# Performance work log

Hardware: AMD Instinct MI355X
Metric: run time of the kernel (lower is better)

## Reference

```python
import jax, jax.numpy as jnp
import numpy as np

# NOBlock config: no_dims_in=(8,8), input_dim=output_dim=128, rank=8, level_diff=1
B, N, V = 4, 2048, 1
G1, G2, C = 8, 8, 128   # in_shape = (8, 8, 128); m = G1*G2 = 64 grid cells per token
M = G1 * G2
R = 8                    # Tucker ranks: [8, 8, 8] in and out (min(dim, rank))
LEVEL_DIFF = 1
GRP = 4 ** LEVEL_DIFF    # quadtree group size for hierarchical residual


def _xavier(key, shape):
    lim = float(np.sqrt(6.0 / (shape[0] + shape[1])))
    return jax.random.uniform(key, shape, jnp.float32, -lim, lim)


def setup_inputs() -> dict:
    key = jax.random.key(0)
    ks = jax.random.split(key, 10)
    x = jax.random.normal(ks[0], (B, N, V, M, C), jnp.float32)
    # core ~ N(0, scale^2), scale = sqrt(2/(fan_in+fan_out)), fan = prod(ranks) = 8^3
    scale = float(np.sqrt(2.0 / (R ** 3 + R ** 3)))
    core = jax.random.normal(ks[1], (R, R, R, R, R, R), jnp.float32) * scale
    out_f0 = _xavier(ks[2], (G1, R))
    out_f1 = _xavier(ks[3], (G2, R))
    out_f2 = _xavier(ks[4], (C, R))
    in_f0 = _xavier(ks[5], (G1, R))
    in_f1 = _xavier(ks[6], (G2, R))
    in_f2 = _xavier(ks[7], (C, R))
    mask = jax.random.bernoulli(ks[8], 0.25, (B, N, M))  # True = masked cell
    return {"x": x, "core": core, "out_f0": out_f0, "out_f1": out_f1,
            "out_f2": out_f2, "in_f0": in_f0, "in_f1": in_f1, "in_f2": in_f2,
            "mask": mask}


def reference(x, core, out_f0, out_f1, out_f2, in_f0, in_f1, in_f2, mask):
    b, n, v = x.shape[:3]
    # --- CrossTuckerLayer: 'bnvade,ABCDEF,oA,pB,qC,aD,dE,eF->bnvopq' ---
    xr = x.reshape(b, n, v, G1, G2, C)
    # project onto in-factor rank spaces
    z = jnp.einsum('bnvade,aD,dE,eF->bnvDEF', xr, in_f0, in_f1, in_f2, optimize=True)
    # core contraction (out-ranks ABC x in-ranks DEF)
    z = jnp.einsum('bnvDEF,ABCDEF->bnvABC', z, core)
    # expand to output dims
    h = jnp.einsum('bnvABC,oA,pB,qC->bnvopq', z, out_f0, out_f1, out_f2, optimize=True)
    h = h.reshape(b, n, v, M, C)
    # residual connection
    h = h + x
    # --- get_residual: hierarchical masked mixing, level_diff = 1 ---
    h4 = h.reshape(b, n * v, M, C)                     # v = 1
    hg = h4.reshape(b, -1, GRP, M, C)                  # [b, n/4, 4, m, c]
    w = (~mask).reshape(b, -1, GRP, M, 1).sum(axis=2, keepdims=True).astype(h.dtype)
    out = (hg / (w + 1e-10)).sum(axis=2)               # [b, n/4, m, c]
    out = out * (w.sum(axis=2) != 0).astype(h.dtype)
    return out
```

## Files before the change

### kernel.cpp

```cpp
#include <hip/hip_runtime.h>
#include <cstdint>
#include <cstddef>


__device__ __forceinline__ float dot4(const float4 a, const float4 b, float s) {
    return fmaf(a.w, b.w, fmaf(a.z, b.z, fmaf(a.y, b.y, fmaf(a.x, b.x, s))));
}

__device__ __forceinline__ unsigned f2bf_pk(float lo, float hi) {
    unsigned ul = __float_as_uint(lo), uh = __float_as_uint(hi);
    ul += 0x7FFFu + ((ul >> 16) & 1u);
    uh += 0x7FFFu + ((uh >> 16) & 1u);
    return (ul >> 16) | (uh & 0xFFFF0000u);
}

__launch_bounds__(256, 4)
__global__ void k1_inproj(const float* __restrict__ x,
                          const float* __restrict__ core,
                          float* __restrict__ coreT,
                          const float* __restrict__ if0,
                          const float* __restrict__ if1,
                          const float* __restrict__ if2,
                          unsigned* __restrict__ xsum_bf,
                          float* __restrict__ zz_ws)
{
    __shared__ float xs[64 * 132];
    __shared__ float s_if2T[8 * 132];
    __shared__ float s_if0[64], s_if1[64];
    float* t1 = xs;
    float* t2 = xs + 512;

    const int t = threadIdx.x;
    const int blk = blockIdx.x;

    if (blk < 64) {
        const int tid = blk * 256 + t;
        const float4* c4 = (const float4*)core;
        float4* cT4 = (float4*)coreT;
        #pragma unroll
        for (int q = 0; q < 4; ++q) {
            const int idx = tid + 16384 * q;
            const int r = idx & 511, k4 = idx >> 9;
            cT4[(size_t)k4 * 512 + r] = c4[(size_t)r * 128 + k4];
        }
        return;
    }
    const int g = blk - 64;

    for (int i = t; i < 1024; i += 256) {
        const int e = i & 127, F = i >> 7;
        s_if2T[F * 132 + e] = if2[e * 8 + F];
    }
    if (t < 64) { s_if0[t] = if0[t]; s_if1[t] = if1[t]; }

    const float4* xg4 = (const float4*)(x + (size_t)g * 4 * 8192);
    float4 acc[8];
    #pragma unroll
    for (int i = 0; i < 8; ++i) acc[i] = xg4[t + 256 * i];
    #pragma unroll
    for (int j = 1; j < 4; ++j) {
        float4 v[8];
        #pragma unroll
        for (int i = 0; i < 8; ++i) v[i] = xg4[(size_t)j * 2048 + t + 256 * i];
        #pragma unroll
        for (int i = 0; i < 8; ++i) {
            acc[i].x += v[i].x; acc[i].y += v[i].y;
            acc[i].z += v[i].z; acc[i].w += v[i].w;
        }
    }
    uint2* xo = (uint2*)xsum_bf + (size_t)g * 2048;
    #pragma unroll
    for (int i = 0; i < 8; ++i) {
        uint2 pk;
        pk.x = f2bf_pk(acc[i].x, acc[i].y);
        pk.y = f2bf_pk(acc[i].z, acc[i].w);
        xo[t + 256 * i] = pk;
    }
    #pragma unroll
    for (int i = 0; i < 8; ++i) {
        const int f4i = t + 256 * i;
        *(float4*)&xs[(f4i >> 5) * 132 + (f4i & 31) * 4] = acc[i];
    }
    __syncthreads();

    float r0, r1;
    #pragma unroll
    for (int h = 0; h < 2; ++h) {
        const int id = t + 256 * h;
        const int m = id >> 3, F = id & 7;
        const float4* xr = (const float4*)(xs + m * 132);
        const float4* wr = (const float4*)(s_if2T + F * 132);
        float s0 = 0.f, s1 = 0.f;
        #pragma unroll
        for (int e4 = 0; e4 < 32; e4 += 2) {
            s0 = dot4(xr[e4],     wr[e4],     s0);
            s1 = dot4(xr[e4 + 1], wr[e4 + 1], s1);
        }
        if (h == 0) r0 = s0 + s1; else r1 = s0 + s1;
    }
    __syncthreads();
    t1[t] = r0;
    t1[t + 256] = r1;
    __syncthreads();

    #pragma unroll
    for (int h = 0; h < 2; ++h) {
        const int id = t + 256 * h;
        const int E = id >> 6, a = (id >> 3) & 7, F = id & 7;
        float s = 0.f;
        #pragma unroll
        for (int d0 = 0; d0 < 8; ++d0) {
            const int d = (d0 + a) & 7;
            s = fmaf(t1[a * 64 + d * 8 + F], s_if1[d * 8 + E], s);
        }
        t2[id] = s;
    }
    __syncthreads();

    #pragma unroll
    for (int h = 0; h < 2; ++h) {
        const int id = t + 256 * h;
        const int D = id >> 6, E = (id >> 3) & 7, F = id & 7;
        float s = 0.f;
        #pragma unroll
        for (int a0 = 0; a0 < 8; ++a0) {
            const int a = (a0 + E) & 7;
            s = fmaf(t2[E * 64 + a * 8 + F], s_if0[a * 8 + D], s);
        }
        zz_ws[(size_t)g * 512 + id] = s;
    }
}

__launch_bounds__(512, 2)
__global__ void k2_core_outproj(const float* __restrict__ coreT,
                                const float* __restrict__ zz_ws,
                                const unsigned* __restrict__ xsum_bf,
                                const float* __restrict__ of0,
                                const float* __restrict__ of1,
                                const float* __restrict__ of2,
                                const int* __restrict__ mask,
                                float* __restrict__ out)
{
    __shared__ float zz[2048];
    __shared__ float z2[2048];
    __shared__ float s_of0T[64], s_of1T[64];
    __shared__ float s_winv[256];
    float* t1 = zz;
    float* t2 = z2;

    const int t = threadIdx.x;
    const size_t g0 = (size_t)blockIdx.x * 4;

    ((float4*)zz)[t] = ((const float4*)(zz_ws + g0 * 512))[t];
    if (t < 64) {
        s_of0T[t] = of0[(t & 7) * 8 + (t >> 3)];
        s_of1T[t] = of1[(t & 7) * 8 + (t >> 3)];
    }
    if (t < 256) {
        const int g = t >> 6, m = t & 63;
        const int* mp = mask + (g0 + g) * 4 * 64 + m;
        int cnt = 0;
        #pragma unroll
        for (int j = 0; j < 4; ++j) cnt += (mp[j * 64] == 0) ? 1 : 0;
        s_winv[t] = cnt ? 1.0f / (float)cnt : 0.0f;
    }
    __syncthreads();

    {
        const float4* cT = (const float4*)coreT;
        const float4* z4 = (const float4*)zz;
        float a0[4] = {0, 0, 0, 0}, a1[4] = {0, 0, 0, 0};
        for (int k4 = 0; k4 < 128; k4 += 2) {
            const float4 c0 = cT[(size_t)k4 * 512 + t];
            const float4 c1 = cT[(size_t)(k4 + 1) * 512 + t];
            #pragma unroll
            for (int g = 0; g < 4; ++g) {
                a0[g] = dot4(c0, z4[g * 128 + k4],     a0[g]);
                a1[g] = dot4(c1, z4[g * 128 + k4 + 1], a1[g]);
            }
        }
        #pragma unroll
        for (int g = 0; g < 4; ++g) z2[g * 512 + t] = a0[g] + a1[g];
    }
    __syncthreads();

    #pragma unroll
    for (int h = 0; h < 4; ++h) {
        const int id2 = t + 512 * h;
        const int g = id2 >> 9, rem = id2 & 511;
        const int o = rem >> 6, Bq = (rem >> 3) & 7, Cr = rem & 7;
        float s = 0.f;
        #pragma unroll
        for (int A = 0; A < 8; ++A)
            s = fmaf(z2[g * 512 + A * 64 + Bq * 8 + Cr], s_of0T[A * 8 + o], s);
        t1[id2] = s;
    }
    __syncthreads();

    #pragma unroll
    for (int h = 0; h < 4; ++h) {
        const int id2 = t + 512 * h;
        const int g = id2 >> 9, rem = id2 & 511;
        const int p = rem >> 6, o = (rem >> 3) & 7, Cr = rem & 7;
        float s = 0.f;
        #pragma unroll
        for (int B0 = 0; B0 < 8; ++B0) {
            const int Bq = (B0 + o) & 7;
            s = fmaf(t1[g * 512 + o * 64 + Bq * 8 + Cr], s_of1T[Bq * 8 + p], s);
        }
        t2[id2] = s;
    }
    __syncthreads();

    float4 w[4][2];
    {
        const int cc = (4 * t) & 127;
        #pragma unroll
        for (int c = 0; c < 4; ++c) {
            w[c][0] = *(const float4*)(of2 + (cc + c) * 8);
            w[c][1] = *(const float4*)(of2 + (cc + c) * 8 + 4);
        }
    }
    float4* out4 = (float4*)out;
    #pragma unroll
    for (int g = 0; g < 4; ++g) {
        const size_t obase = (g0 + g) * 2048;
        const uint2* xb = (const uint2*)xsum_bf + obase;
        uint2 xp[4];
        #pragma unroll
        for (int i = 0; i < 4; ++i) xp[i] = xb[t + 512 * i];
        #pragma unroll
        for (int i = 0; i < 4; ++i) {
            const int m = (t >> 5) + 16 * i;
            const int o = m >> 3, p = m & 7;
            const float wv = s_winv[g * 64 + m];
            const int base = g * 512 + p * 64 + o * 8;
            const float4 v0 = *(const float4*)(t2 + base);
            const float4 v1 = *(const float4*)(t2 + base + 4);
            const float rx = __uint_as_float(xp[i].x << 16);
            const float ry = __uint_as_float(xp[i].x & 0xFFFF0000u);
            const float rz = __uint_as_float(xp[i].y << 16);
            const float rw = __uint_as_float(xp[i].y & 0xFFFF0000u);
            float4 r;
            r.x = dot4(v1, w[0][1], dot4(v0, w[0][0], rx));
            r.y = dot4(v1, w[1][1], dot4(v0, w[1][0], ry));
            r.z = dot4(v1, w[2][1], dot4(v0, w[2][0], rz));
            r.w = dot4(v1, w[3][1], dot4(v0, w[3][0], rw));
            r.x *= wv; r.y *= wv; r.z *= wv; r.w *= wv;
            out4[obase + t + 512 * i] = r;
        }
    }
}

__launch_bounds__(256, 3)
__global__ void noblock_fused(const float* __restrict__ x,
                              const float* __restrict__ core,
                              const float* __restrict__ of0,
                              const float* __restrict__ of1,
                              const float* __restrict__ of2,
                              const float* __restrict__ if0,
                              const float* __restrict__ if1,
                              const float* __restrict__ if2,
                              const int* __restrict__ mask,
                              float* __restrict__ out)
{
    __shared__ float xs[64 * 132];
    __shared__ float t1[512];
    __shared__ float t2[512];
    __shared__ float zz[2 * 512];
    __shared__ float z2[2 * 512];
    __shared__ float s_if2T[8 * 132];
    __shared__ float s_if0[64], s_if1[64];
    __shared__ float s_of0T[64], s_of1T[64];
    __shared__ float s_winv[128];

    const int t = threadIdx.x;
    const int blk = blockIdx.x;

    for (int i = t; i < 1024; i += 256) {
        const int e = i & 127, F = i >> 7;
        s_if2T[F * 132 + e] = if2[e * 8 + F];
    }
    if (t < 64) {
        s_if0[t] = if0[t];
        s_if1[t] = if1[t];
        s_of0T[t] = of0[(t & 7) * 8 + (t >> 3)];
        s_of1T[t] = of1[(t & 7) * 8 + (t >> 3)];
    }
    if (t < 128) {
        const int g = t >> 6, mm = t & 63;
        const int* mp = mask + ((size_t)(blk * 2 + g) * 4) * 64 + mm;
        int cnt = 0;
        #pragma unroll
        for (int j = 0; j < 4; ++j) cnt += (mp[j * 64] == 0) ? 1 : 0;
        s_winv[t] = cnt ? 1.0f / (float)cnt : 0.0f;
    }

    float4 acc[2][8];
    const float4* xg4 = (const float4*)(x + (size_t)blk * 8 * 8192);
    #pragma unroll
    for (int g = 0; g < 2; ++g)
        #pragma unroll
        for (int i = 0; i < 8; ++i)
            acc[g][i] = xg4[(size_t)(g * 4) * 2048 + t + 256 * i];
    #pragma unroll
    for (int j = 1; j < 4; ++j) {
        #pragma unroll
        for (int g = 0; g < 2; ++g) {
            float4 v[8];
            #pragma unroll
            for (int i = 0; i < 8; ++i)
                v[i] = xg4[(size_t)(g * 4 + j) * 2048 + t + 256 * i];
            #pragma unroll
            for (int i = 0; i < 8; ++i) {
                acc[g][i].x += v[i].x; acc[g][i].y += v[i].y;
                acc[g][i].z += v[i].z; acc[g][i].w += v[i].w;
            }
        }
    }

    #pragma unroll
    for (int g = 0; g < 2; ++g) {
        #pragma unroll
        for (int i = 0; i < 8; ++i) {
            const int f4i = t + 256 * i;
            *(float4*)&xs[(f4i >> 5) * 132 + (f4i & 31) * 4] = acc[g][i];
        }
        __syncthreads();
        #pragma unroll
        for (int h = 0; h < 2; ++h) {
            const int id = t + 256 * h;
            const int m = id >> 3, F = id & 7;
            const float4* xr = (const float4*)(xs + m * 132);
            const float4* wr = (const float4*)(s_if2T + F * 132);
            float s0 = 0.f, s1 = 0.f;
            #pragma unroll
            for (int e4 = 0; e4 < 32; e4 += 2) {
                s0 = dot4(xr[e4],     wr[e4],     s0);
                s1 = dot4(xr[e4 + 1], wr[e4 + 1], s1);
            }
            t1[id] = s0 + s1;
        }
        __syncthreads();
        #pragma unroll
        for (int h = 0; h < 2; ++h) {
            const int id = t + 256 * h;
            const int E = id >> 6, a = (id >> 3) & 7, F = id & 7;
            float s = 0.f;
            #pragma unroll
            for (int d0 = 0; d0 < 8; ++d0) {
                const int d = (d0 + a) & 7;
                s = fmaf(t1[a * 64 + d * 8 + F], s_if1[d * 8 + E], s);
            }
            t2[id] = s;
        }
        __syncthreads();
        #pragma unroll
        for (int h = 0; h < 2; ++h) {
            const int id = t + 256 * h;
            const int D = id >> 6, E = (id >> 3) & 7, F = id & 7;
            float s = 0.f;
            #pragma unroll
            for (int a0 = 0; a0 < 8; ++a0) {
                const int a = (a0 + E) & 7;
                s = fmaf(t2[E * 64 + a * 8 + F], s_if0[a * 8 + D], s);
            }
            zz[g * 512 + id] = s;
        }
        __syncthreads();
    }

    {
        const float4* cr0 = (const float4*)(core + (size_t)t * 512);
        const float4* cr1 = (const float4*)(core + (size_t)(t + 256) * 512);
        const float4* z4 = (const float4*)zz;
        float a0[2] = {0.f, 0.f}, a1[2] = {0.f, 0.f};
        for (int kk = 0; kk < 128; ++kk) {
            const float4 c0 = cr0[kk], c1 = cr1[kk];
            #pragma unroll
            for (int g = 0; g < 2; ++g) {
                const float4 zv = z4[g * 128 + kk];
                a0[g] = dot4(c0, zv, a0[g]);
                a1[g] = dot4(c1, zv, a1[g]);
            }
        }
        #pragma unroll
        for (int g = 0; g < 2; ++g) {
            z2[g * 512 + t]       = a0[g];
            z2[g * 512 + t + 256] = a1[g];
        }
    }
    __syncthreads();

    float4 w[4][2];
    {
        const int cc = (4 * t) & 127;
        #pragma unroll
        for (int c = 0; c < 4; ++c) {
            w[c][0] = *(const float4*)(of2 + (cc + c) * 8);
            w[c][1] = *(const float4*)(of2 + (cc + c) * 8 + 4);
        }
    }

    float4* out4 = (float4*)out;
    #pragma unroll
    for (int g = 0; g < 2; ++g) {
        #pragma unroll
        for (int h = 0; h < 2; ++h) {
            const int id = t + 256 * h;
            const int o = id >> 6, Bq = (id >> 3) & 7, Cr = id & 7;
            float s = 0.f;
            #pragma unroll
            for (int A = 0; A < 8; ++A)
                s = fmaf(z2[g * 512 + A * 64 + Bq * 8 + Cr], s_of0T[A * 8 + o], s);
            t1[id] = s;
        }
        __syncthreads();
        #pragma unroll
        for (int h = 0; h < 2; ++h) {
            const int id = t + 256 * h;
            const int p = id >> 6, o = (id >> 3) & 7, Cr = id & 7;
            float s = 0.f;
            #pragma unroll
            for (int B0 = 0; B0 < 8; ++B0) {
                const int Bq = (B0 + o) & 7;
                s = fmaf(t1[o * 64 + Bq * 8 + Cr], s_of1T[Bq * 8 + p], s);
            }
            t2[id] = s;
        }
        __syncthreads();
        #pragma unroll
        for (int i = 0; i < 8; ++i) {
            const int m = (t >> 5) + 8 * i;
            const int o = m >> 3, p = m & 7;
            const float wv = s_winv[g * 64 + m];
            const int base = p * 64 + o * 8;
            const float4 v0 = *(const float4*)(t2 + base);
            const float4 v1 = *(const float4*)(t2 + base + 4);
            float4 r;
            r.x = dot4(v1, w[0][1], dot4(v0, w[0][0], acc[g][i].x));
            r.y = dot4(v1, w[1][1], dot4(v0, w[1][0], acc[g][i].y));
            r.z = dot4(v1, w[2][1], dot4(v0, w[2][0], acc[g][i].z));
            r.w = dot4(v1, w[3][1], dot4(v0, w[3][0], acc[g][i].w));
            r.x *= wv; r.y *= wv; r.z *= wv; r.w *= wv;
            out4[(size_t)(blk * 2 + g) * 2048 + t + 256 * i] = r;
        }
        __syncthreads();
    }
}

extern "C" void kernel_launch(void* const* d_in, const int* in_sizes, int n_in,
                              void* d_out, int out_size, void* d_ws, size_t ws_size,
                              hipStream_t stream) {
    const float* x    = (const float*)d_in[0];
    const float* core = (const float*)d_in[1];
    const float* of0  = (const float*)d_in[2];
    const float* of1  = (const float*)d_in[3];
    const float* of2  = (const float*)d_in[4];
    const float* if0  = (const float*)d_in[5];
    const float* if1  = (const float*)d_in[6];
    const float* if2  = (const float*)d_in[7];
    const int* mask   = (const int*)d_in[8];
    float* out = (float*)d_out;

    const size_t CORE_T_BYTES = (size_t)512 * 512 * 4;
    const size_t ZZ_BYTES     = (size_t)2048 * 512 * 4;
    const size_t XS_BYTES     = (size_t)2048 * 8192 * 2;

    if (d_ws && ws_size >= CORE_T_BYTES + ZZ_BYTES + XS_BYTES) {
        float* coreT    = (float*)d_ws;
        float* zz_ws    = (float*)((char*)d_ws + CORE_T_BYTES);
        unsigned* xs_bf = (unsigned*)((char*)d_ws + CORE_T_BYTES + ZZ_BYTES);
        k1_inproj<<<dim3(2112), dim3(256), 0, stream>>>(
            x, core, coreT, if0, if1, if2, xs_bf, zz_ws);
        k2_core_outproj<<<dim3(512), dim3(512), 0, stream>>>(
            coreT, zz_ws, xs_bf, of0, of1, of2, mask, out);
    } else {
        noblock_fused<<<dim3(1024), dim3(256), 0, stream>>>(
            x, core, of0, of1, of2, if0, if1, if2, mask, out);
    }
}
```

Measured before the change: 111.8 us.

## Fuse input projection into core/output kernel, split core transpose into its own launch

The input-projection stage (x group sum, bf16 residual store, Tucker in-projection) moves into the main kernel. Each 512-thread block now processes its 4 groups sequentially into shared memory, so the zz intermediate no longer round-trips through global memory. Core transposition becomes a tiny separate kernel. The trade-off is a loop of 4 groups with several syncs per group inside one block, and grid-level parallelism for the x reads drops from 2048 blocks to 512 blocks, which could reduce memory-level parallelism.

New measurement: 107.6 us. 3.8% less time.

```diff
diff --git a/kernel.cpp b/kernel.cpp
--- a/kernel.cpp
+++ b/kernel.cpp
@@ -14,145 +14,49 @@
     return (ul >> 16) | (uh & 0xFFFF0000u);
 }
 
-__launch_bounds__(256, 4)
-__global__ void k1_inproj(const float* __restrict__ x,
-                          const float* __restrict__ core,
-                          float* __restrict__ coreT,
-                          const float* __restrict__ if0,
-                          const float* __restrict__ if1,
-                          const float* __restrict__ if2,
-                          unsigned* __restrict__ xsum_bf,
-                          float* __restrict__ zz_ws)
+__global__ void transpose_core(const float* __restrict__ core,
+                               float* __restrict__ coreT) {
+    const int tid = blockIdx.x * 256 + threadIdx.x;
+    const int r = tid & 511, k4 = tid >> 9;
+    ((float4*)coreT)[(size_t)k4 * 512 + r] =
+        ((const float4*)core)[(size_t)r * 128 + k4];
+}
+
+__launch_bounds__(512, 2)
+__global__ void noblock_main(const float* __restrict__ x,
+                             const float* __restrict__ coreT,
+                             const float* __restrict__ of0,
+                             const float* __restrict__ of1,
+                             const float* __restrict__ of2,
+                             const float* __restrict__ if0,
+                             const float* __restrict__ if1,
+                             const float* __restrict__ if2,
+                             const int* __restrict__ mask,
+                             unsigned* __restrict__ xsum_bf,
+                             float* __restrict__ out)
 {
     __shared__ float xs[64 * 132];
+    __shared__ float zz[2048];
+    __shared__ float z2[2048];
     __shared__ float s_if2T[8 * 132];
     __shared__ float s_if0[64], s_if1[64];
+    __shared__ float s_of0T[64], s_of1T[64];
+    __shared__ float s_winv[256];
     float* t1 = xs;
     float* t2 = xs + 512;
+    float* t1d = zz;
+    float* t2d = z2;
 
     const int t = threadIdx.x;
-    const int blk = blockIdx.x;
-
-    if (blk < 64) {
-        const int tid = blk * 256 + t;
-        const float4* c4 = (const float4*)core;
-        float4* cT4 = (float4*)coreT;
-        #pragma unroll
-        for (int q = 0; q < 4; ++q) {
-            const int idx = tid + 16384 * q;
-            const int r = idx & 511, k4 = idx >> 9;
-            cT4[(size_t)k4 * 512 + r] = c4[(size_t)r * 128 + k4];
-        }
-        return;
-    }
-    const int g = blk - 64;
-
-    for (int i = t; i < 1024; i += 256) {
+    const size_t g0 = (size_t)blockIdx.x * 4;
+
+    for (int i = t; i < 1024; i += 512) {
         const int e = i & 127, F = i >> 7;
         s_if2T[F * 132 + e] = if2[e * 8 + F];
     }
-    if (t < 64) { s_if0[t] = if0[t]; s_if1[t] = if1[t]; }
-
-    const float4* xg4 = (const float4*)(x + (size_t)g * 4 * 8192);
-    float4 acc[8];
-    #pragma unroll
-    for (int i = 0; i < 8; ++i) acc[i] = xg4[t + 256 * i];
-    #pragma unroll
-    for (int j = 1; j < 4; ++j) {
-        float4 v[8];
-        #pragma unroll
-        for (int i = 0; i < 8; ++i) v[i] = xg4[(size_t)j * 2048 + t + 256 * i];
-        #pragma unroll
-        for (int i = 0; i < 8; ++i) {
-            acc[i].x += v[i].x; acc[i].y += v[i].y;
-            acc[i].z += v[i].z; acc[i].w += v[i].w;
-        }
-    }
-    uint2* xo = (uint2*)xsum_bf + (size_t)g * 2048;
-    #pragma unroll
-    for (int i = 0; i < 8; ++i) {
-        uint2 pk;
-        pk.x = f2bf_pk(acc[i].x, acc[i].y);
-        pk.y = f2bf_pk(acc[i].z, acc[i].w);
-        xo[t + 256 * i] = pk;
-    }
-    #pragma unroll
-    for (int i = 0; i < 8; ++i) {
-        const int f4i = t + 256 * i;
-        *(float4*)&xs[(f4i >> 5) * 132 + (f4i & 31) * 4] = acc[i];
-    }
-    __syncthreads();
-
-    float r0, r1;
-    #pragma unroll
-    for (int h = 0; h < 2; ++h) {
-        const int id = t + 256 * h;
-        const int m = id >> 3, F = id & 7;
-        const float4* xr = (const float4*)(xs + m * 132);
-        const float4* wr = (const float4*)(s_if2T + F * 132);
-        float s0 = 0.f, s1 = 0.f;
-        #pragma unroll
-        for (int e4 = 0; e4 < 32; e4 += 2) {
-            s0 = dot4(xr[e4],     wr[e4],     s0);
-            s1 = dot4(xr[e4 + 1], wr[e4 + 1], s1);
-        }
-        if (h == 0) r0 = s0 + s1; else r1 = s0 + s1;
-    }
-    __syncthreads();
-    t1[t] = r0;
-    t1[t + 256] = r1;
-    __syncthreads();
-
-    #pragma unroll
-    for (int h = 0; h < 2; ++h) {
-        const int id = t + 256 * h;
-        const int E = id >> 6, a = (id >> 3) & 7, F = id & 7;
-        float s = 0.f;
-        #pragma unroll
-        for (int d0 = 0; d0 < 8; ++d0) {
-            const int d = (d0 + a) & 7;
-            s = fmaf(t1[a * 64 + d * 8 + F], s_if1[d * 8 + E], s);
-        }
-        t2[id] = s;
-    }
-    __syncthreads();
-
-    #pragma unroll
-    for (int h = 0; h < 2; ++h) {
-        const int id = t + 256 * h;
-        const int D = id >> 6, E = (id >> 3) & 7, F = id & 7;
-        float s = 0.f;
-        #pragma unroll
-        for (int a0 = 0; a0 < 8; ++a0) {
-            const int a = (a0 + E) & 7;
-            s = fmaf(t2[E * 64 + a * 8 + F], s_if0[a * 8 + D], s);
-        }
-        zz_ws[(size_t)g * 512 + id] = s;
-    }
-}
-
-__launch_bounds__(512, 2)
-__global__ void k2_core_outproj(const float* __restrict__ coreT,
-                                const float* __restrict__ zz_ws,
-                                const unsigned* __restrict__ xsum_bf,
-                                const float* __restrict__ of0,
-                                const float* __restrict__ of1,
-                                const float* __restrict__ of2,
-                                const int* __restrict__ mask,
-                                float* __restrict__ out)
-{
-    __shared__ float zz[2048];
-    __shared__ float z2[2048];
-    __shared__ float s_of0T[64], s_of1T[64];
-    __shared__ float s_winv[256];
-    float* t1 = zz;
-    float* t2 = z2;
-
-    const int t = threadIdx.x;
-    const size_t g0 = (size_t)blockIdx.x * 4;
-
-    ((float4*)zz)[t] = ((const float4*)(zz_ws + g0 * 512))[t];
     if (t < 64) {
+        s_if0[t] = if0[t];
+        s_if1[t] = if1[t];
         s_of0T[t] = of0[(t & 7) * 8 + (t >> 3)];
         s_of1T[t] = of1[(t & 7) * 8 + (t >> 3)];
     }
@@ -164,7 +68,80 @@
         for (int j = 0; j < 4; ++j) cnt += (mp[j * 64] == 0) ? 1 : 0;
         s_winv[t] = cnt ? 1.0f / (float)cnt : 0.0f;
     }
-    __syncthreads();
+
+    #pragma unroll 1
+    for (int g = 0; g < 4; ++g) {
+        const float4* xg4 = (const float4*)x + (g0 + g) * 8192;
+        float4 v[4][4];
+        #pragma unroll
+        for (int j = 0; j < 4; ++j)
+            #pragma unroll
+            for (int i = 0; i < 4; ++i)
+                v[j][i] = xg4[(size_t)j * 2048 + t + 512 * i];
+        float4 acc[4];
+        #pragma unroll
+        for (int i = 0; i < 4; ++i) {
+            acc[i].x = (v[0][i].x + v[1][i].x) + (v[2][i].x + v[3][i].x);
+            acc[i].y = (v[0][i].y + v[1][i].y) + (v[2][i].y + v[3][i].y);
+            acc[i].z = (v[0][i].z + v[1][i].z) + (v[2][i].z + v[3][i].z);
+            acc[i].w = (v[0][i].w + v[1][i].w) + (v[2][i].w + v[3][i].w);
+        }
+        uint2* xo = (uint2*)xsum_bf + (g0 + g) * 2048;
+        #pragma unroll
+        for (int i = 0; i < 4; ++i) {
+            uint2 pk;
+            pk.x = f2bf_pk(acc[i].x, acc[i].y);
+            pk.y = f2bf_pk(acc[i].z, acc[i].w);
+            xo[t + 512 * i] = pk;
+        }
+        #pragma unroll
+        for (int i = 0; i < 4; ++i) {
+            const int f4i = t + 512 * i;
+            *(float4*)&xs[(f4i >> 5) * 132 + (f4i & 31) * 4] = acc[i];
+        }
+        __syncthreads();
+
+        float r0;
+        {
+            const int m = t >> 3, F = t & 7;
+            const float4* xr = (const float4*)(xs + m * 132);
+            const float4* wr = (const float4*)(s_if2T + F * 132);
+            float s0 = 0.f, s1 = 0.f;
+            #pragma unroll
+            for (int e4 = 0; e4 < 32; e4 += 2) {
+                s0 = dot4(xr[e4],     wr[e4],     s0);
+                s1 = dot4(xr[e4 + 1], wr[e4 + 1], s1);
+            }
+            r0 = s0 + s1;
+        }
+        __syncthreads();
+        t1[t] = r0;
+        __syncthreads();
+
+        {
+            const int E = t >> 6, a = (t >> 3) & 7, F = t & 7;
+            float s = 0.f;
+            #pragma unroll
+            for (int d0 = 0; d0 < 8; ++d0) {
+                const int d = (d0 + a) & 7;
+                s = fmaf(t1[a * 64 + d * 8 + F], s_if1[d * 8 + E], s);
+            }
+            t2[t] = s;
+        }
+        __syncthreads();
+
+        {
+            const int D = t >> 6, E = (t >> 3) & 7, F = t & 7;
+            float s = 0.f;
+            #pragma unroll
+            for (int a0 = 0; a0 < 8; ++a0) {
+                const int a = (a0 + E) & 7;
+                s = fmaf(t2[E * 64 + a * 8 + F], s_if0[a * 8 + D], s);
+            }
+            zz[g * 512 + t] = s;
+        }
+        __syncthreads();
+    }
 
     {
         const float4* cT = (const float4*)coreT;
@@ -193,7 +170,7 @@
         #pragma unroll
         for (int A = 0; A < 8; ++A)
             s = fmaf(z2[g * 512 + A * 64 + Bq * 8 + Cr], s_of0T[A * 8 + o], s);
-        t1[id2] = s;
+        t1d[id2] = s;
     }
     __syncthreads();
 
@@ -206,9 +183,9 @@
         #pragma unroll
         for (int B0 = 0; B0 < 8; ++B0) {
             const int Bq = (B0 + o) & 7;
-            s = fmaf(t1[g * 512 + o * 64 + Bq * 8 + Cr], s_of1T[Bq * 8 + p], s);
-        }
-        t2[id2] = s;
+            s = fmaf(t1d[g * 512 + o * 64 + Bq * 8 + Cr], s_of1T[Bq * 8 + p], s);
+        }
+        t2d[id2] = s;
     }
     __syncthreads();
 
@@ -235,8 +212,8 @@
             const int o = m >> 3, p = m & 7;
             const float wv = s_winv[g * 64 + m];
             const int base = g * 512 + p * 64 + o * 8;
-            const float4 v0 = *(const float4*)(t2 + base);
-            const float4 v1 = *(const float4*)(t2 + base + 4);
+            const float4 v0 = *(const float4*)(t2d + base);
+            const float4 v1 = *(const float4*)(t2d + base + 4);
             const float rx = __uint_as_float(xp[i].x << 16);
             const float ry = __uint_as_float(xp[i].x & 0xFFFF0000u);
             const float rz = __uint_as_float(xp[i].y << 16);
@@ -464,17 +441,14 @@
     float* out = (float*)d_out;
 
     const size_t CORE_T_BYTES = (size_t)512 * 512 * 4;
-    const size_t ZZ_BYTES     = (size_t)2048 * 512 * 4;
     const size_t XS_BYTES     = (size_t)2048 * 8192 * 2;
 
-    if (d_ws && ws_size >= CORE_T_BYTES + ZZ_BYTES + XS_BYTES) {
+    if (d_ws && ws_size >= CORE_T_BYTES + XS_BYTES) {
         float* coreT    = (float*)d_ws;
-        float* zz_ws    = (float*)((char*)d_ws + CORE_T_BYTES);
-        unsigned* xs_bf = (unsigned*)((char*)d_ws + CORE_T_BYTES + ZZ_BYTES);
-        k1_inproj<<<dim3(2112), dim3(256), 0, stream>>>(
-            x, core, coreT, if0, if1, if2, xs_bf, zz_ws);
-        k2_core_outproj<<<dim3(512), dim3(512), 0, stream>>>(
-            coreT, zz_ws, xs_bf, of0, of1, of2, mask, out);
+        unsigned* xs_bf = (unsigned*)((char*)d_ws + CORE_T_BYTES);
+        transpose_core<<<dim3(256), dim3(256), 0, stream>>>(core, coreT);
+        noblock_main<<<dim3(512), dim3(512), 0, stream>>>(
+            x, coreT, of0, of1, of2, if0, if1, if2, mask, xs_bf, out);
     } else {
         noblock_fused<<<dim3(1024), dim3(256), 0, stream>>>(
             x, core, of0, of1, of2, if0, if1, if2, mask, out);
```
